# Optimization experiments

Measured on AMD Instinct MI355X. Metric: run time of the kernel, lower is better.

The kernel has to match this reference:

```python
import jax, jax.numpy as jnp
import numpy as np
import itertools


def _comb_indices(F, k):
    # Flattened combination indices: for each of C(F,k) combinations, its k
    # member feature ids, concatenated. Row i of the original one-hot crmatrix
    # has a single 1 at column idx[i], so x @ crmatrix^T == gather by idx.
    return np.fromiter(itertools.chain(*itertools.combinations(range(F), k)),
                       dtype=np.int32)


def setup_inputs() -> dict:
    key = jax.random.key(0)
    x = jax.random.normal(key, (32, 4096, 32), dtype=jnp.float32)  # [B, T, F]
    return {"x": x, "k": 2}


def reference(x, k):
    F = x.shape[2]
    idx = jnp.asarray(_comb_indices(F, k))          # [ncr] = [k * C(F,k)]
    # Faithful to K.dot(x, crmatrix) with one-hot crmatrix: a feature gather.
    return jnp.take(x, idx, axis=2)                 # [B, T, ncr]
```

## Files before the change

kernel.cpp:

```cpp
#include <hip/hip_runtime.h>


#define FDIM 32
#define NCR 992
#define G_PER_ROW 248
#define BLOCK 256
#define GRID 2048

typedef float f32x4 __attribute__((ext_vector_type(4)));

__global__ __launch_bounds__(BLOCK, 8)
void comb_gather_kernel(const float* __restrict__ x,
                        float* __restrict__ out,
                        int nrows) {
    const int tid = threadIdx.x;
    const int b   = blockIdx.x;

    {
        const int r = tid;
        size_t row = (size_t)b + (size_t)r * GRID;
        if (tid < 64 && row < (size_t)nrows) {
            float w = x[row * FDIM];
            asm volatile("" :: "v"(w));
        }
    }

    if (tid >= G_PER_ROW) return;

    int feat[4];
    {
        const int c0 = 2 * tid;
        float s = sqrtf(3969.0f - 8.0f * (float)c0);
        int i0 = (int)((63.0f - s) * 0.5f);
        if (i0 < 0) i0 = 0;
        int st0  = (i0 * (63 - i0)) >> 1;
        int stn0 = ((i0 + 1) * (62 - i0)) >> 1;
        if (stn0 <= c0) { i0++; st0 = stn0; stn0 = ((i0 + 1) * (62 - i0)) >> 1; }
        else if (st0 > c0) { i0--; stn0 = st0; st0 = (i0 * (63 - i0)) >> 1; }
        feat[0] = i0;
        feat[1] = c0 - st0 + i0 + 1;
        const int c1 = c0 + 1;
        int i1 = i0, st1 = st0;
        if (stn0 <= c1) { i1 = i0 + 1; st1 = stn0; }
        feat[2] = i1;
        feat[3] = c1 - st1 + i1 + 1;
    }

    const float* rowp = x + (size_t)b * FDIM;
    f32x4*       outp = reinterpret_cast<f32x4*>(out + (size_t)b * NCR) + tid;
    const size_t xstep = (size_t)GRID * FDIM;
    const size_t ostep = (size_t)GRID * (NCR / 4);

    const int iters = (nrows - b + GRID - 1) / GRID;

    #pragma unroll 4
    for (int r = 0; r < iters; ++r) {
        f32x4 v;
        v.x = rowp[feat[0]];
        v.y = rowp[feat[1]];
        v.z = rowp[feat[2]];
        v.w = rowp[feat[3]];
        __builtin_nontemporal_store(v, outp);
        rowp += xstep;
        outp += ostep;
    }
}

extern "C" void kernel_launch(void* const* d_in, const int* in_sizes, int n_in,
                              void* d_out, int out_size, void* d_ws, size_t ws_size,
                              hipStream_t stream) {
    const float* x  = (const float*)d_in[0];
    float* out      = (float*)d_out;
    int nrows = in_sizes[0] / FDIM;
    hipLaunchKernelGGL(comb_gather_kernel, dim3(GRID), dim3(BLOCK), 0, stream,
                       x, out, nrows);
}
```

Before: 103.5 us.

## Flatten gather into grid-stride loop over all output vec4 groups

The old mapping had each block own a strided set of rows with 248 of 256 threads active. It is replaced by a flat grid-stride loop over every output float4 group, so all threads do work and each step writes a contiguous output span. The combination-index math (sqrt and corrections) and a divide by 248 now run every iteration instead of once per thread. The early prefetch of row heads is also removed.

```diff
diff --git a/kernel.cpp b/kernel.cpp
--- a/kernel.cpp
+++ b/kernel.cpp
@@ -13,23 +13,18 @@
 void comb_gather_kernel(const float* __restrict__ x,
                         float* __restrict__ out,
                         int nrows) {
-    const int tid = threadIdx.x;
-    const int b   = blockIdx.x;
+    const unsigned total   = (unsigned)nrows * G_PER_ROW;
+    const unsigned nthread = GRID * BLOCK;
+    unsigned G = blockIdx.x * BLOCK + threadIdx.x;
 
-    {
-        const int r = tid;
-        size_t row = (size_t)b + (size_t)r * GRID;
-        if (tid < 64 && row < (size_t)nrows) {
-            float w = x[row * FDIM];
-            asm volatile("" :: "v"(w));
-        }
-    }
+    f32x4* outv = reinterpret_cast<f32x4*>(out);
 
-    if (tid >= G_PER_ROW) return;
+    #pragma unroll 4
+    for (; G < total; G += nthread) {
+        const unsigned row = G / G_PER_ROW;
+        const unsigned g   = G - row * G_PER_ROW;
 
-    int feat[4];
-    {
-        const int c0 = 2 * tid;
+        const int c0 = 2 * (int)g;
         float s = sqrtf(3969.0f - 8.0f * (float)c0);
         int i0 = (int)((63.0f - s) * 0.5f);
         if (i0 < 0) i0 = 0;
@@ -37,32 +32,22 @@
         int stn0 = ((i0 + 1) * (62 - i0)) >> 1;
         if (stn0 <= c0) { i0++; st0 = stn0; stn0 = ((i0 + 1) * (62 - i0)) >> 1; }
         else if (st0 > c0) { i0--; stn0 = st0; st0 = (i0 * (63 - i0)) >> 1; }
-        feat[0] = i0;
-        feat[1] = c0 - st0 + i0 + 1;
+        const int f0 = i0;
+        const int f1 = c0 - st0 + i0 + 1;
         const int c1 = c0 + 1;
         int i1 = i0, st1 = st0;
         if (stn0 <= c1) { i1 = i0 + 1; st1 = stn0; }
-        feat[2] = i1;
-        feat[3] = c1 - st1 + i1 + 1;
-    }
+        const int f2 = i1;
+        const int f3 = c1 - st1 + i1 + 1;
 
-    const float* rowp = x + (size_t)b * FDIM;
-    f32x4*       outp = reinterpret_cast<f32x4*>(out + (size_t)b * NCR) + tid;
-    const size_t xstep = (size_t)GRID * FDIM;
-    const size_t ostep = (size_t)GRID * (NCR / 4);
+        const float* rowp = x + (size_t)row * FDIM;
+        f32x4 v;
+        v.x = rowp[f0];
+        v.y = rowp[f1];
+        v.z = rowp[f2];
+        v.w = rowp[f3];
 
-    const int iters = (nrows - b + GRID - 1) / GRID;
-
-    #pragma unroll 4
-    for (int r = 0; r < iters; ++r) {
-        f32x4 v;
-        v.x = rowp[feat[0]];
-        v.y = rowp[feat[1]];
-        v.z = rowp[feat[2]];
-        v.w = rowp[feat[3]];
-        __builtin_nontemporal_store(v, outp);
-        rowp += xstep;
-        outp += ostep;
+        __builtin_nontemporal_store(v, outv + G);
     }
 }
 
```

New measurement: 104.5 us. No clear change (+1.0%).
